# Kernel tuning notes

Measured on AMD Instinct MI355X. Metric: run time of the kernel, lower is better.

The kernel has to match this reference:

```python
import jax, jax.numpy as jnp
import numpy as np

FEAT = 1024
DEPTH = 3
NUM_SCALES = 5
N_NODES = 2 ** DEPTH - 1  # 7
N_LEAVES = 2 ** DEPTH     # 8
HID = 64
LN_EPS = 1e-5


def setup_inputs() -> dict:
    key = jax.random.key(0)
    ks = jax.random.split(key, 16)
    B, D = 8192, 4096
    s = 0.02
    return {
        "features": jax.random.normal(ks[0], (B, FEAT), jnp.float32),
        "logits": jax.random.normal(ks[1], (NUM_SCALES, B, D), jnp.float32),
        # all 7 tree nodes stacked (identical shapes at every level)
        "tw1": jax.random.normal(ks[2], (N_NODES, HID, FEAT), jnp.float32) * s,
        "tb1": jnp.zeros((N_NODES, HID), jnp.float32),
        "tg": jnp.ones((N_NODES, HID), jnp.float32),   # LayerNorm gamma
        "tbn": jnp.zeros((N_NODES, HID), jnp.float32),  # LayerNorm beta
        "tw2": jax.random.normal(ks[3], (N_NODES, 2, HID), jnp.float32) * s,
        "tb2": jnp.zeros((N_NODES, 2), jnp.float32),
        # leaf_to_scale: Linear(8, 10) -> GELU -> Linear(10, 5)
        "lw1": jax.random.normal(ks[4], (NUM_SCALES * 2, N_LEAVES), jnp.float32) * s,
        "lb1": jnp.zeros((NUM_SCALES * 2,), jnp.float32),
        "lw2": jax.random.normal(ks[5], (NUM_SCALES, NUM_SCALES * 2), jnp.float32) * s,
        "lb2": jnp.zeros((NUM_SCALES,), jnp.float32),
        # direct_gate: Linear(1024, 256) -> GELU -> Linear(256, 5)
        "dw1": jax.random.normal(ks[6], (FEAT // 4, FEAT), jnp.float32) * s,
        "db1": jnp.zeros((FEAT // 4,), jnp.float32),
        "dw2": jax.random.normal(ks[7], (NUM_SCALES, FEAT // 4), jnp.float32) * s,
        "db2": jnp.zeros((NUM_SCALES,), jnp.float32),
        "combine_weight": jnp.asarray(0.7, jnp.float32),
    }


def _forward(features, logits, tw1, tb1, tg, tbn, tw2, tb2,
             lw1, lb1, lw2, lb2, dw1, db1, dw2, db2, combine_weight):
    B = features.shape[0]
    # all tree nodes in one batched GEMM: [B, 7, 64]
    h = jnp.einsum("bf,nhf->bnh", features, tw1) + tb1
    mu = jnp.mean(h, axis=-1, keepdims=True)
    var = jnp.var(h, axis=-1, keepdims=True)
    h = (h - mu) / jnp.sqrt(var + LN_EPS) * tg + tbn
    h = jax.nn.gelu(h, approximate=False)  # torch GELU default = exact
    node_logits = jnp.einsum("bnh,noh->bno", h, tw2) + tb2  # [B, 7, 2]
    node_probs = jax.nn.softmax(node_logits / 0.5, axis=-1)
    # traverse levels: node ordering is BFS (level 0: node 0, level 1: 1..2, level 2: 3..6)
    p = jnp.ones((B, 1), features.dtype)
    offset = 0
    for level in range(DEPTH):
        n = 2 ** level
        pr = node_probs[:, offset:offset + n]          # [B, n, 2]
        p = (p[:, :, None] * pr).reshape(B, 2 * n)      # children interleaved L,R
        offset += n
    leaf_probs = p  # [B, 8]
    t = jax.nn.gelu(leaf_probs @ lw1.T + lb1, approximate=False)
    tree_gates = jax.nn.softmax(t @ lw2.T + lb2, axis=-1)
    d = jax.nn.gelu(features @ dw1.T + db1, approximate=False)
    direct_gates = jax.nn.softmax(d @ dw2.T + db2, axis=-1)
    w = jax.nn.sigmoid(combine_weight)
    gates = w * tree_gates + (1.0 - w) * direct_gates
    gates = gates / jnp.sum(gates, axis=-1, keepdims=True)
    # weighted combine over scales: memory-bound reduction over 5 large tensors
    combined = jnp.einsum("bs,sbd->bd", gates, logits)
    return combined, gates


def reference(features, logits, tw1, tb1, tg, tbn, tw2, tb2,
              lw1, lb1, lw2, lb2, dw1, db1, dw2, db2, combine_weight):
    return _forward(features, logits, tw1, tb1, tg, tbn, tw2, tb2,
                    lw1, lb1, lw2, lb2, dw1, db1, dw2, db2, combine_weight)
```

## Files before the change

kernel.cpp:

```cpp
#include <hip/hip_runtime.h>
#include <math.h>

#define B_SZ   8192
#define FEATN  1024
#define DCOL   4096
#define NS     5
#define NN     7
#define HIDN   64
#define NTREE  448
#define NDIR   256
#define NTOT   704


#define BM 128
#define BN 64
#define BK 16
#define LDA 132
#define LDB 68

typedef float f32x4_t __attribute__((ext_vector_type(4)));

__device__ inline float gelu_exact(float x) {
    return 0.5f * x * (1.f + erff(x * 0.70710678118654752f));
}

__global__ __launch_bounds__(256) void htg_gemm_fused(
    const float* __restrict__ A, const float* __restrict__ tw1,
    const float* __restrict__ dw1,
    const float* __restrict__ tb1, const float* __restrict__ tg,
    const float* __restrict__ tbn, const float* __restrict__ tw2,
    const float* __restrict__ tb2,
    const float* __restrict__ db1, const float* __restrict__ dw2,
    float* __restrict__ np_out, float* __restrict__ dpart_out)
{
    __shared__ float As[BK * LDA];
    __shared__ float Bs[BK * LDB];
    const int tid = threadIdx.x;
    const int bm0 = blockIdx.x * BM;
    const int bn0 = blockIdx.y * BN;
    const float* Wsrc = (bn0 < NTREE) ? (tw1 + (size_t)bn0 * FEATN)
                                      : (dw1 + (size_t)(bn0 - NTREE) * FEATN);
    const int ty  = tid >> 4;
    const int tx  = tid & 15;
    const int lr  = tid >> 2;
    const int lc4 = tid & 3;

    float acc[8][4];
#pragma unroll
    for (int i = 0; i < 8; ++i)
#pragma unroll
        for (int j = 0; j < 4; ++j) acc[i][j] = 0.f;

    float4 aR0, aR1, bR;
    {
        const float* Ap = A + (size_t)(bm0 + lr) * FEATN + lc4 * 4;
        aR0 = *(const float4*)(Ap);
        aR1 = *(const float4*)(Ap + (size_t)64 * FEATN);
        bR  = *(const float4*)(Wsrc + (size_t)lr * FEATN + lc4 * 4);
    }
    const int KT = FEATN / BK;
    for (int kt = 0; kt < KT; ++kt) {
        {
            float av0[4] = {aR0.x, aR0.y, aR0.z, aR0.w};
            float av1[4] = {aR1.x, aR1.y, aR1.z, aR1.w};
            float bv[4]  = {bR.x,  bR.y,  bR.z,  bR.w};
#pragma unroll
            for (int j = 0; j < 4; ++j) {
                As[(lc4 * 4 + j) * LDA + lr]      = av0[j];
                As[(lc4 * 4 + j) * LDA + lr + 64] = av1[j];
                Bs[(lc4 * 4 + j) * LDB + lr]      = bv[j];
            }
        }
        __syncthreads();
        if (kt + 1 < KT) {
            const int k0 = (kt + 1) * BK;
            const float* Ap = A + (size_t)(bm0 + lr) * FEATN + k0 + lc4 * 4;
            aR0 = *(const float4*)(Ap);
            aR1 = *(const float4*)(Ap + (size_t)64 * FEATN);
            bR  = *(const float4*)(Wsrc + (size_t)lr * FEATN + k0 + lc4 * 4);
        }
#pragma unroll
        for (int kk = 0; kk < BK; ++kk) {
            float4 a0 = *(const float4*)&As[kk * LDA + ty * 8];
            float4 a1 = *(const float4*)&As[kk * LDA + ty * 8 + 4];
            float4 b  = *(const float4*)&Bs[kk * LDB + tx * 4];
            float av[8] = {a0.x, a0.y, a0.z, a0.w, a1.x, a1.y, a1.z, a1.w};
            float bv[4] = {b.x, b.y, b.z, b.w};
#pragma unroll
            for (int i = 0; i < 8; ++i)
#pragma unroll
                for (int j = 0; j < 4; ++j)
                    acc[i][j] = fmaf(av[i], bv[j], acc[i][j]);
        }
        __syncthreads();
    }

    const int ib = blockIdx.y;
    if (ib < NN) {
        const int n = ib;
        const int col = tx * 4;
        const float4 tb1v = *(const float4*)&tb1[n * HIDN + col];
        const float4 tgv  = *(const float4*)&tg [n * HIDN + col];
        const float4 tbnv = *(const float4*)&tbn[n * HIDN + col];
        const float4 w2av = *(const float4*)&tw2[(n * 2 + 0) * HIDN + col];
        const float4 w2bv = *(const float4*)&tw2[(n * 2 + 1) * HIDN + col];
        const float b2a = tb2[n * 2], b2b = tb2[n * 2 + 1];
        const float tb1a[4] = {tb1v.x, tb1v.y, tb1v.z, tb1v.w};
        const float tga[4]  = {tgv.x,  tgv.y,  tgv.z,  tgv.w};
        const float tbna[4] = {tbnv.x, tbnv.y, tbnv.z, tbnv.w};
        const float w2aa[4] = {w2av.x, w2av.y, w2av.z, w2av.w};
        const float w2ba[4] = {w2bv.x, w2bv.y, w2bv.z, w2bv.w};
#pragma unroll
        for (int i = 0; i < 8; ++i) {
            float x[4]; float s = 0.f, sq = 0.f;
#pragma unroll
            for (int j = 0; j < 4; ++j) {
                x[j] = acc[i][j] + tb1a[j];
                s += x[j];
                sq = fmaf(x[j], x[j], sq);
            }
#pragma unroll
            for (int o = 8; o > 0; o >>= 1) {
                s  += __shfl_xor(s,  o, 64);
                sq += __shfl_xor(sq, o, 64);
            }
            const float mu  = s * (1.f / 64.f);
            const float var = sq * (1.f / 64.f) - mu * mu;
            const float rs  = rsqrtf(var + 1e-5f);
            float o0 = 0.f, o1 = 0.f;
#pragma unroll
            for (int j = 0; j < 4; ++j) {
                const float g = gelu_exact((x[j] - mu) * rs * tga[j] + tbna[j]);
                o0 = fmaf(g, w2aa[j], o0);
                o1 = fmaf(g, w2ba[j], o1);
            }
#pragma unroll
            for (int o = 8; o > 0; o >>= 1) {
                o0 += __shfl_xor(o0, o, 64);
                o1 += __shfl_xor(o1, o, 64);
            }
            o0 += b2a; o1 += b2b;
            const float p0 = 1.f / (1.f + expf(2.f * (o1 - o0)));
            if (tx == 0) np_out[(size_t)(bm0 + ty * 8 + i) * NN + n] = p0;
        }
    } else {
        const int cb  = ib - NN;
        const int col = cb * HIDN + tx * 4;
        const float4 dbv = *(const float4*)&db1[col];
        const float dba[4] = {dbv.x, dbv.y, dbv.z, dbv.w};
        float w2[NS][4];
#pragma unroll
        for (int s5 = 0; s5 < NS; ++s5) {
            const float4 v = *(const float4*)&dw2[s5 * NDIR + col];
            w2[s5][0] = v.x; w2[s5][1] = v.y; w2[s5][2] = v.z; w2[s5][3] = v.w;
        }
#pragma unroll
        for (int i = 0; i < 8; ++i) {
            float part[NS] = {0.f, 0.f, 0.f, 0.f, 0.f};
#pragma unroll
            for (int j = 0; j < 4; ++j) {
                const float d = gelu_exact(acc[i][j] + dba[j]);
#pragma unroll
                for (int s5 = 0; s5 < NS; ++s5) part[s5] = fmaf(d, w2[s5][j], part[s5]);
            }
#pragma unroll
            for (int o = 8; o > 0; o >>= 1)
#pragma unroll
                for (int s5 = 0; s5 < NS; ++s5) part[s5] += __shfl_xor(part[s5], o, 64);
            if (tx == 0) {
                const size_t r = bm0 + ty * 8 + i;
#pragma unroll
                for (int s5 = 0; s5 < NS; ++s5)
                    dpart_out[r * 20 + cb * NS + s5] = part[s5];
            }
        }
    }
}

__device__ inline void softmax5(float* v) {
    float m = v[0];
#pragma unroll
    for (int s = 1; s < NS; ++s) m = fmaxf(m, v[s]);
    float sum = 0.f;
#pragma unroll
    for (int s = 0; s < NS; ++s) { v[s] = expf(v[s] - m); sum += v[s]; }
    const float inv = 1.f / sum;
#pragma unroll
    for (int s = 0; s < NS; ++s) v[s] *= inv;
}

__global__ __launch_bounds__(256) void htg_gates_lite(
    const float* __restrict__ np, const float* __restrict__ dpart,
    const float* __restrict__ lw1, const float* __restrict__ lb1,
    const float* __restrict__ lw2, const float* __restrict__ lb2,
    const float* __restrict__ db2, const float* __restrict__ cw,
    float* __restrict__ gates_out)
{
    const int b = blockIdx.x * 256 + threadIdx.x;
    float np0[NN], np1[NN];
#pragma unroll
    for (int n = 0; n < NN; ++n) {
        np0[n] = np[(size_t)b * NN + n];
        np1[n] = 1.f - np0[n];
    }
    float lp[8];
#pragma unroll
    for (int leaf = 0; leaf < 8; ++leaf) {
        const int c0 = (leaf >> 2) & 1, c1 = (leaf >> 1) & 1, c2 = leaf & 1;
        const float v0 = c0 ? np1[0] : np0[0];
        const float v1 = c1 ? np1[1 + c0] : np0[1 + c0];
        const float v2 = c2 ? np1[3 + 2 * c0 + c1] : np0[3 + 2 * c0 + c1];
        lp[leaf] = v0 * v1 * v2;
    }
    float t[10];
#pragma unroll
    for (int j = 0; j < 10; ++j) {
        float a = lb1[j];
#pragma unroll
        for (int leaf = 0; leaf < 8; ++leaf) a = fmaf(lp[leaf], lw1[j * 8 + leaf], a);
        t[j] = gelu_exact(a);
    }
    float tgt[NS];
#pragma unroll
    for (int s = 0; s < NS; ++s) {
        float a = lb2[s];
#pragma unroll
        for (int j = 0; j < 10; ++j) a = fmaf(t[j], lw2[s * 10 + j], a);
        tgt[s] = a;
    }
    softmax5(tgt);
    float dgt[NS];
#pragma unroll
    for (int s = 0; s < NS; ++s) {
        float a = db2[s];
#pragma unroll
        for (int cb = 0; cb < 4; ++cb) a += dpart[(size_t)b * 20 + cb * NS + s];
        dgt[s] = a;
    }
    softmax5(dgt);
    const float w = 1.f / (1.f + expf(-cw[0]));
    float g5[NS]; float sum = 0.f;
#pragma unroll
    for (int s = 0; s < NS; ++s) {
        g5[s] = fmaf(w, tgt[s] - dgt[s], dgt[s]);
        sum += g5[s];
    }
    const float inv = 1.f / sum;
#pragma unroll
    for (int s = 0; s < NS; ++s) gates_out[(size_t)b * NS + s] = g5[s] * inv;
}

__global__ __launch_bounds__(256) void htg_combine(
    const float* __restrict__ logits, const float* __restrict__ gates,
    float* __restrict__ out)
{
    const int b = blockIdx.x;
    float g[NS];
#pragma unroll
    for (int s = 0; s < NS; ++s) g[s] = gates[(size_t)b * NS + s];
    const f32x4_t* lp = (const f32x4_t*)logits;
    f32x4_t* op = (f32x4_t*)out;
    const size_t rowbase = (size_t)b * (DCOL / 4);
#pragma unroll
    for (int u = 0; u < 4; ++u) {
        const size_t idx = rowbase + u * 256 + threadIdx.x;
        f32x4_t a = (f32x4_t)(0.f);
#pragma unroll
        for (int s = 0; s < NS; ++s) {
            const f32x4_t v = __builtin_nontemporal_load(&lp[(size_t)s * B_SZ * (DCOL / 4) + idx]);
            a.x = fmaf(g[s], v.x, a.x);
            a.y = fmaf(g[s], v.y, a.y);
            a.z = fmaf(g[s], v.z, a.z);
            a.w = fmaf(g[s], v.w, a.w);
        }
        __builtin_nontemporal_store(a, &op[idx]);
    }
}

extern "C" void kernel_launch(void* const* d_in, const int* in_sizes, int n_in,
                              void* d_out, int out_size, void* d_ws, size_t ws_size,
                              hipStream_t stream) {
    const float* features = (const float*)d_in[0];
    const float* logits   = (const float*)d_in[1];
    const float* tw1      = (const float*)d_in[2];
    const float* tb1      = (const float*)d_in[3];
    const float* tg       = (const float*)d_in[4];
    const float* tbn      = (const float*)d_in[5];
    const float* tw2      = (const float*)d_in[6];
    const float* tb2      = (const float*)d_in[7];
    const float* lw1      = (const float*)d_in[8];
    const float* lb1      = (const float*)d_in[9];
    const float* lw2      = (const float*)d_in[10];
    const float* lb2      = (const float*)d_in[11];
    const float* dw1      = (const float*)d_in[12];
    const float* db1      = (const float*)d_in[13];
    const float* dw2      = (const float*)d_in[14];
    const float* db2      = (const float*)d_in[15];
    const float* cw       = (const float*)d_in[16];

    float* out   = (float*)d_out;
    float* gates = out + (size_t)B_SZ * DCOL;

    const size_t scratch_bytes = (size_t)B_SZ * 27 * sizeof(float);
    float* scratch   = (ws_size >= scratch_bytes) ? (float*)d_ws : (float*)d_out;
    float* np_buf    = scratch;
    float* dpart_buf = scratch + (size_t)B_SZ * NN;

    dim3 gemm_grid(B_SZ / BM, NTOT / BN);
    htg_gemm_fused<<<gemm_grid, 256, 0, stream>>>(features, tw1, dw1,
                                                  tb1, tg, tbn, tw2, tb2,
                                                  db1, dw2, np_buf, dpart_buf);

    htg_gates_lite<<<B_SZ / 256, 256, 0, stream>>>(np_buf, dpart_buf,
                                                   lw1, lb1, lw2, lb2, db2, cw,
                                                   gates);

    htg_combine<<<B_SZ, 256, 0, stream>>>(logits, gates, out);
}
```

Measured before the change: 1.059 ms.

## Replace FP32 SIMT GEMM with split-bf16 3-term MFMA GEMM

Adds a conversion kernel that splits features and the stacked tree/direct weights into bf16 high and low halves. The fused GEMM is rewritten to use 16x16x32 bf16 MFMA instructions with three products (hi*hi, hi*lo, lo*hi) to approximate FP32 accuracy, reading operands directly from global memory without LDS staging. The epilogue is remapped to the MFMA accumulator layout. It adds an extra pass over the 32MB feature matrix and the scratch writes, and assumes the workspace can hold the split copies.

```diff
diff --git a/kernel.cpp b/kernel.cpp
--- a/kernel.cpp
+++ b/kernel.cpp
@@ -12,166 +12,189 @@
 #define NTOT   704
 
 
-#define BM 128
-#define BN 64
-#define BK 16
-#define LDA 132
-#define LDB 68
-
-typedef float f32x4_t __attribute__((ext_vector_type(4)));
+typedef float  f32x4_t  __attribute__((ext_vector_type(4)));
+typedef short  bf16x8_t __attribute__((ext_vector_type(8)));
+typedef unsigned short u16;
 
 __device__ inline float gelu_exact(float x) {
     return 0.5f * x * (1.f + erff(x * 0.70710678118654752f));
 }
-
-__global__ __launch_bounds__(256) void htg_gemm_fused(
-    const float* __restrict__ A, const float* __restrict__ tw1,
+__device__ inline u16 f32_to_bf16_rne(float x) {
+    unsigned u = __float_as_uint(x);
+    return (u16)((u + 0x7FFFu + ((u >> 16) & 1u)) >> 16);
+}
+
+__global__ __launch_bounds__(256) void htg_convert(
+    const float* __restrict__ feat, const float* __restrict__ tw1,
     const float* __restrict__ dw1,
+    u16* __restrict__ Ah, u16* __restrict__ Al,
+    u16* __restrict__ Wh, u16* __restrict__ Wl)
+{
+    const int NF4 = (B_SZ * FEATN) / 4;
+    const int NT4 = (NTREE * FEATN) / 4;
+    const int NW4 = (NTOT * FEATN) / 4;
+    const int total = NF4 + NW4;
+    for (int i = blockIdx.x * 256 + threadIdx.x; i < total; i += gridDim.x * 256) {
+        float4 v;
+        u16 *hq, *lq; int o;
+        if (i < NF4) {
+            v = ((const float4*)feat)[i];
+            hq = Ah; lq = Al; o = i * 4;
+        } else {
+            const int wi = i - NF4;
+            v = (wi < NT4) ? ((const float4*)tw1)[wi] : ((const float4*)dw1)[wi - NT4];
+            hq = Wh; lq = Wl; o = wi * 4;
+        }
+        const float xs[4] = {v.x, v.y, v.z, v.w};
+        ushort4 hv, lv;
+        u16 h[4], l[4];
+#pragma unroll
+        for (int j = 0; j < 4; ++j) {
+            h[j] = f32_to_bf16_rne(xs[j]);
+            const float fhi = __uint_as_float(((unsigned)h[j]) << 16);
+            l[j] = f32_to_bf16_rne(xs[j] - fhi);
+        }
+        hv.x = h[0]; hv.y = h[1]; hv.z = h[2]; hv.w = h[3];
+        lv.x = l[0]; lv.y = l[1]; lv.z = l[2]; lv.w = l[3];
+        *(ushort4*)(hq + o) = hv;
+        *(ushort4*)(lq + o) = lv;
+    }
+}
+
+__global__ __launch_bounds__(256) void htg_gemm_mfma(
+    const u16* __restrict__ Ah, const u16* __restrict__ Al,
+    const u16* __restrict__ Wh, const u16* __restrict__ Wl,
     const float* __restrict__ tb1, const float* __restrict__ tg,
     const float* __restrict__ tbn, const float* __restrict__ tw2,
     const float* __restrict__ tb2,
     const float* __restrict__ db1, const float* __restrict__ dw2,
     float* __restrict__ np_out, float* __restrict__ dpart_out)
 {
-    __shared__ float As[BK * LDA];
-    __shared__ float Bs[BK * LDB];
-    const int tid = threadIdx.x;
-    const int bm0 = blockIdx.x * BM;
-    const int bn0 = blockIdx.y * BN;
-    const float* Wsrc = (bn0 < NTREE) ? (tw1 + (size_t)bn0 * FEATN)
-                                      : (dw1 + (size_t)(bn0 - NTREE) * FEATN);
-    const int ty  = tid >> 4;
-    const int tx  = tid & 15;
-    const int lr  = tid >> 2;
-    const int lc4 = tid & 3;
-
-    float acc[8][4];
-#pragma unroll
-    for (int i = 0; i < 8; ++i)
-#pragma unroll
-        for (int j = 0; j < 4; ++j) acc[i][j] = 0.f;
-
-    float4 aR0, aR1, bR;
-    {
-        const float* Ap = A + (size_t)(bm0 + lr) * FEATN + lc4 * 4;
-        aR0 = *(const float4*)(Ap);
-        aR1 = *(const float4*)(Ap + (size_t)64 * FEATN);
-        bR  = *(const float4*)(Wsrc + (size_t)lr * FEATN + lc4 * 4);
-    }
-    const int KT = FEATN / BK;
-    for (int kt = 0; kt < KT; ++kt) {
-        {
-            float av0[4] = {aR0.x, aR0.y, aR0.z, aR0.w};
-            float av1[4] = {aR1.x, aR1.y, aR1.z, aR1.w};
-            float bv[4]  = {bR.x,  bR.y,  bR.z,  bR.w};
-#pragma unroll
-            for (int j = 0; j < 4; ++j) {
-                As[(lc4 * 4 + j) * LDA + lr]      = av0[j];
-                As[(lc4 * 4 + j) * LDA + lr + 64] = av1[j];
-                Bs[(lc4 * 4 + j) * LDB + lr]      = bv[j];
-            }
-        }
-        __syncthreads();
-        if (kt + 1 < KT) {
-            const int k0 = (kt + 1) * BK;
-            const float* Ap = A + (size_t)(bm0 + lr) * FEATN + k0 + lc4 * 4;
-            aR0 = *(const float4*)(Ap);
-            aR1 = *(const float4*)(Ap + (size_t)64 * FEATN);
-            bR  = *(const float4*)(Wsrc + (size_t)lr * FEATN + k0 + lc4 * 4);
-        }
-#pragma unroll
-        for (int kk = 0; kk < BK; ++kk) {
-            float4 a0 = *(const float4*)&As[kk * LDA + ty * 8];
-            float4 a1 = *(const float4*)&As[kk * LDA + ty * 8 + 4];
-            float4 b  = *(const float4*)&Bs[kk * LDB + tx * 4];
-            float av[8] = {a0.x, a0.y, a0.z, a0.w, a1.x, a1.y, a1.z, a1.w};
-            float bv[4] = {b.x, b.y, b.z, b.w};
-#pragma unroll
-            for (int i = 0; i < 8; ++i)
-#pragma unroll
-                for (int j = 0; j < 4; ++j)
-                    acc[i][j] = fmaf(av[i], bv[j], acc[i][j]);
-        }
-        __syncthreads();
+    const int tid  = threadIdx.x;
+    const int wave = tid >> 6;
+    const int lane = tid & 63;
+    const int cidx = lane & 15;
+    const int kgrp = (lane >> 4) * 8;
+    const int bm0  = blockIdx.x * 128;
+    const int bn0  = blockIdx.y * 64;
+
+    const size_t a0 = (size_t)(bm0 + wave * 32 + cidx) * FEATN;
+    const size_t a1 = a0 + (size_t)16 * FEATN;
+    size_t woff[4];
+#pragma unroll
+    for (int n = 0; n < 4; ++n)
+        woff[n] = (size_t)(bn0 + n * 16 + cidx) * FEATN;
+
+    f32x4_t acc[2][4];
+#pragma unroll
+    for (int m = 0; m < 2; ++m)
+#pragma unroll
+        for (int n = 0; n < 4; ++n) acc[m][n] = (f32x4_t)(0.f);
+
+#pragma unroll 2
+    for (int k0 = 0; k0 < FEATN; k0 += 32) {
+        const int ko = k0 + kgrp;
+        const bf16x8_t a0h = *(const bf16x8_t*)(Ah + a0 + ko);
+        const bf16x8_t a0l = *(const bf16x8_t*)(Al + a0 + ko);
+        const bf16x8_t a1h = *(const bf16x8_t*)(Ah + a1 + ko);
+        const bf16x8_t a1l = *(const bf16x8_t*)(Al + a1 + ko);
+#pragma unroll
+        for (int n = 0; n < 4; ++n) {
+            const bf16x8_t wh = *(const bf16x8_t*)(Wh + woff[n] + ko);
+            const bf16x8_t wl = *(const bf16x8_t*)(Wl + woff[n] + ko);
+            acc[0][n] = __builtin_amdgcn_mfma_f32_16x16x32_bf16(a0l, wh, acc[0][n], 0, 0, 0);
+            acc[0][n] = __builtin_amdgcn_mfma_f32_16x16x32_bf16(a0h, wl, acc[0][n], 0, 0, 0);
+            acc[0][n] = __builtin_amdgcn_mfma_f32_16x16x32_bf16(a0h, wh, acc[0][n], 0, 0, 0);
+            acc[1][n] = __builtin_amdgcn_mfma_f32_16x16x32_bf16(a1l, wh, acc[1][n], 0, 0, 0);
+            acc[1][n] = __builtin_amdgcn_mfma_f32_16x16x32_bf16(a1h, wl, acc[1][n], 0, 0, 0);
+            acc[1][n] = __builtin_amdgcn_mfma_f32_16x16x32_bf16(a1h, wh, acc[1][n], 0, 0, 0);
+        }
     }
 
     const int ib = blockIdx.y;
     if (ib < NN) {
-        const int n = ib;
-        const int col = tx * 4;
-        const float4 tb1v = *(const float4*)&tb1[n * HIDN + col];
-        const float4 tgv  = *(const float4*)&tg [n * HIDN + col];
-        const float4 tbnv = *(const float4*)&tbn[n * HIDN + col];
-        const float4 w2av = *(const float4*)&tw2[(n * 2 + 0) * HIDN + col];
-        const float4 w2bv = *(const float4*)&tw2[(n * 2 + 1) * HIDN + col];
-        const float b2a = tb2[n * 2], b2b = tb2[n * 2 + 1];
-        const float tb1a[4] = {tb1v.x, tb1v.y, tb1v.z, tb1v.w};
-        const float tga[4]  = {tgv.x,  tgv.y,  tgv.z,  tgv.w};
-        const float tbna[4] = {tbnv.x, tbnv.y, tbnv.z, tbnv.w};
-        const float w2aa[4] = {w2av.x, w2av.y, w2av.z, w2av.w};
-        const float w2ba[4] = {w2bv.x, w2bv.y, w2bv.z, w2bv.w};
-#pragma unroll
-        for (int i = 0; i < 8; ++i) {
-            float x[4]; float s = 0.f, sq = 0.f;
-#pragma unroll
-            for (int j = 0; j < 4; ++j) {
-                x[j] = acc[i][j] + tb1a[j];
-                s += x[j];
-                sq = fmaf(x[j], x[j], sq);
+        const int n0 = ib;
+        float tb1a[4], tga[4], tbna[4], w2aa[4], w2ba[4];
+#pragma unroll
+        for (int n = 0; n < 4; ++n) {
+            const int col = n * 16 + cidx;
+            tb1a[n] = tb1[n0 * HIDN + col];
+            tga[n]  = tg [n0 * HIDN + col];
+            tbna[n] = tbn[n0 * HIDN + col];
+            w2aa[n] = tw2[(n0 * 2 + 0) * HIDN + col];
+            w2ba[n] = tw2[(n0 * 2 + 1) * HIDN + col];
+        }
+        const float b2a = tb2[n0 * 2], b2b = tb2[n0 * 2 + 1];
+#pragma unroll
+        for (int mt = 0; mt < 2; ++mt) {
+#pragma unroll
+            for (int r = 0; r < 4; ++r) {
+                float x[4]; float s = 0.f, sq = 0.f;
+#pragma unroll
+                for (int n = 0; n < 4; ++n) {
+                    x[n] = acc[mt][n][r] + tb1a[n];
+                    s += x[n];
+                    sq = fmaf(x[n], x[n], sq);
+                }
+#pragma unroll
+                for (int o = 8; o > 0; o >>= 1) {
+                    s  += __shfl_xor(s,  o, 64);
+                    sq += __shfl_xor(sq, o, 64);
+                }
+                const float mu  = s * (1.f / 64.f);
+                const float var = sq * (1.f / 64.f) - mu * mu;
+                const float rs  = rsqrtf(var + 1e-5f);
+                float o0 = 0.f, o1 = 0.f;
+#pragma unroll
+                for (int n = 0; n < 4; ++n) {
+                    const float g = gelu_exact((x[n] - mu) * rs * tga[n] + tbna[n]);
+                    o0 = fmaf(g, w2aa[n], o0);
+                    o1 = fmaf(g, w2ba[n], o1);
+                }
+#pragma unroll
+                for (int o = 8; o > 0; o >>= 1) {
+                    o0 += __shfl_xor(o0, o, 64);
+                    o1 += __shfl_xor(o1, o, 64);
+                }
+                o0 += b2a; o1 += b2b;
+                const float p0 = 1.f / (1.f + expf(2.f * (o1 - o0)));
+                if (cidx == 0) {
+                    const int row = bm0 + wave * 32 + mt * 16 + (lane >> 4) * 4 + r;
+                    np_out[(size_t)row * NN + n0] = p0;
+                }
             }
-#pragma unroll
-            for (int o = 8; o > 0; o >>= 1) {
-                s  += __shfl_xor(s,  o, 64);
-                sq += __shfl_xor(sq, o, 64);
-            }
-            const float mu  = s * (1.f / 64.f);
-            const float var = sq * (1.f / 64.f) - mu * mu;
-            const float rs  = rsqrtf(var + 1e-5f);
-            float o0 = 0.f, o1 = 0.f;
-#pragma unroll
-            for (int j = 0; j < 4; ++j) {
-                const float g = gelu_exact((x[j] - mu) * rs * tga[j] + tbna[j]);
-                o0 = fmaf(g, w2aa[j], o0);
-                o1 = fmaf(g, w2ba[j], o1);
-            }
-#pragma unroll
-            for (int o = 8; o > 0; o >>= 1) {
-                o0 += __shfl_xor(o0, o, 64);
-                o1 += __shfl_xor(o1, o, 64);
-            }
-            o0 += b2a; o1 += b2b;
-            const float p0 = 1.f / (1.f + expf(2.f * (o1 - o0)));
-            if (tx == 0) np_out[(size_t)(bm0 + ty * 8 + i) * NN + n] = p0;
         }
     } else {
-        const int cb  = ib - NN;
-        const int col = cb * HIDN + tx * 4;
-        const float4 dbv = *(const float4*)&db1[col];
-        const float dba[4] = {dbv.x, dbv.y, dbv.z, dbv.w};
-        float w2[NS][4];
-#pragma unroll
-        for (int s5 = 0; s5 < NS; ++s5) {
-            const float4 v = *(const float4*)&dw2[s5 * NDIR + col];
-            w2[s5][0] = v.x; w2[s5][1] = v.y; w2[s5][2] = v.z; w2[s5][3] = v.w;
-        }
-#pragma unroll
-        for (int i = 0; i < 8; ++i) {
-            float part[NS] = {0.f, 0.f, 0.f, 0.f, 0.f};
-#pragma unroll
-            for (int j = 0; j < 4; ++j) {
-                const float d = gelu_exact(acc[i][j] + dba[j]);
-#pragma unroll
-                for (int s5 = 0; s5 < NS; ++s5) part[s5] = fmaf(d, w2[s5][j], part[s5]);
-            }
-#pragma unroll
-            for (int o = 8; o > 0; o >>= 1)
-#pragma unroll
-                for (int s5 = 0; s5 < NS; ++s5) part[s5] += __shfl_xor(part[s5], o, 64);
-            if (tx == 0) {
-                const size_t r = bm0 + ty * 8 + i;
-#pragma unroll
-                for (int s5 = 0; s5 < NS; ++s5)
-                    dpart_out[r * 20 + cb * NS + s5] = part[s5];
+        const int cb = ib - NN;
+        float dba[4], w2d[NS][4];
+#pragma unroll
+        for (int n = 0; n < 4; ++n) {
+            const int col = cb * HIDN + n * 16 + cidx;
+            dba[n] = db1[col];
+#pragma unroll
+            for (int s5 = 0; s5 < NS; ++s5) w2d[s5][n] = dw2[s5 * NDIR + col];
+        }
+#pragma unroll
+        for (int mt = 0; mt < 2; ++mt) {
+#pragma unroll
+            for (int r = 0; r < 4; ++r) {
+                float part[NS] = {0.f, 0.f, 0.f, 0.f, 0.f};
+#pragma unroll
+                for (int n = 0; n < 4; ++n) {
+                    const float d = gelu_exact(acc[mt][n][r] + dba[n]);
+#pragma unroll
+                    for (int s5 = 0; s5 < NS; ++s5) part[s5] = fmaf(d, w2d[s5][n], part[s5]);
+                }
+#pragma unroll
+                for (int o = 8; o > 0; o >>= 1)
+#pragma unroll
+                    for (int s5 = 0; s5 < NS; ++s5) part[s5] += __shfl_xor(part[s5], o, 64);
+                if (cidx == 0) {
+                    const size_t row = bm0 + wave * 32 + mt * 16 + (lane >> 4) * 4 + r;
+#pragma unroll
+                    for (int s5 = 0; s5 < NS; ++s5)
+                        dpart_out[row * 20 + cb * NS + s5] = part[s5];
+                }
             }
         }
     }
@@ -301,15 +324,24 @@
     float* out   = (float*)d_out;
     float* gates = out + (size_t)B_SZ * DCOL;
 
-    const size_t scratch_bytes = (size_t)B_SZ * 27 * sizeof(float);
-    float* scratch   = (ws_size >= scratch_bytes) ? (float*)d_ws : (float*)d_out;
-    float* np_buf    = scratch;
-    float* dpart_buf = scratch + (size_t)B_SZ * NN;
-
-    dim3 gemm_grid(B_SZ / BM, NTOT / BN);
-    htg_gemm_fused<<<gemm_grid, 256, 0, stream>>>(features, tw1, dw1,
-                                                  tb1, tg, tbn, tw2, tb2,
-                                                  db1, dw2, np_buf, dpart_buf);
+    const size_t nA = (size_t)B_SZ * FEATN;
+    const size_t nW = (size_t)NTOT * FEATN;
+    const size_t scratch_bytes = (2 * nA + 2 * nW) * sizeof(u16)
+                               + (size_t)B_SZ * 27 * sizeof(float);
+    char* scratch = (ws_size >= scratch_bytes) ? (char*)d_ws : (char*)d_out;
+    u16* Ah = (u16*)scratch;
+    u16* Al = Ah + nA;
+    u16* Wh = Al + nA;
+    u16* Wl = Wh + nW;
+    float* np_buf    = (float*)(Wl + nW);
+    float* dpart_buf = np_buf + (size_t)B_SZ * NN;
+
+    htg_convert<<<2048, 256, 0, stream>>>(features, tw1, dw1, Ah, Al, Wh, Wl);
+
+    dim3 gemm_grid(B_SZ / 128, NTOT / 64);
+    htg_gemm_mfma<<<gemm_grid, 256, 0, stream>>>(Ah, Al, Wh, Wl,
+                                                 tb1, tg, tbn, tw2, tb2,
+                                                 db1, dw2, np_buf, dpart_buf);
 
     htg_gates_lite<<<B_SZ / 256, 256, 0, stream>>>(np_buf, dpart_buf,
                                                    lw1, lb1, lw2, lb2, db2, cw,
```

Result: no change. 1.042 ms (-1.5%).
